# Kernel tuning notes

Measured on AMD Instinct MI355X. Metric: run time of the kernel, lower is better.

## Reference

```python
import jax, jax.numpy as jnp
import numpy as np

DIM = 256
NUM_HEADS = 8


def setup_inputs() -> dict:
    key = jax.random.key(0)
    ks = jax.random.split(key, 8)
    B, H, W = 2, 64, 64
    s = 0.02
    return {
        "query": jax.random.normal(ks[0], (B, H, W, DIM), jnp.float32),
        "sim": jax.random.normal(ks[1], (B, H, W, DIM), jnp.float32),
        "Wq": jax.random.normal(ks[2], (DIM, DIM), jnp.float32) * s,
        "bq": jnp.zeros((DIM,), jnp.float32),
        "Wkv": jax.random.normal(ks[3], (DIM, 2 * DIM), jnp.float32) * s,
        "bkv": jnp.zeros((2 * DIM,), jnp.float32),
        "Wp": jax.random.normal(ks[4], (DIM, DIM), jnp.float32) * s,
        "bp": jnp.zeros((DIM,), jnp.float32),
    }


def reference(query, sim, Wq, bq, Wkv, bkv, Wp, bp):
    B, H, W, dim = query.shape
    nh = NUM_HEADS
    dh = dim // nh
    scale = dh ** (-0.5)
    S = H * W

    # projections
    q = (query.reshape(B, S, dim) @ Wq + bq).reshape(B, S, nh, dh)
    kv = (sim.reshape(B, S, dim) @ Wkv + bkv).reshape(B, S, 2, nh, dh)
    k = kv[:, :, 0]  # [B,S,nh,dh]
    v = kv[:, :, 1]

    # attention: scores [B,nh,S,S]
    attn = jnp.einsum('bqhd,bkhd->bhqk', q * scale, k)
    attn = jax.nn.softmax(attn, axis=-1)
    x = jnp.einsum('bhqk,bkhd->bqhd', attn, v)  # [B,S,nh,dh]
    x = x.reshape(B, H, W, dim)
    return x @ Wp + bp
```

## Files before the change

kernel.cpp:

```cpp
#include <hip/hip_runtime.h>
#include <hip/hip_bf16.h>
#include <math.h>


#define SCALE 0.17677669529663687f
#define LOG2E 1.4426950408889634f

typedef __attribute__((ext_vector_type(8))) short short8;
typedef __attribute__((ext_vector_type(8))) _Float16 half8;
typedef __attribute__((ext_vector_type(4))) float f32x4;

static __device__ __forceinline__ unsigned short f2bf(float x) {
    union { float f; unsigned int u; } v; v.f = x;
    unsigned int r = v.u + 0x7fff + ((v.u >> 16) & 1);
    return (unsigned short)(r >> 16);
}
static __device__ __forceinline__ float bf2f(unsigned short h) {
    union { unsigned int u; float f; } v; v.u = ((unsigned int)h) << 16;
    return v.f;
}
static __device__ __forceinline__ float fexp2(float x) {
#if __has_builtin(__builtin_amdgcn_exp2f)
    return __builtin_amdgcn_exp2f(x);
#else
    float r; asm("v_exp_f32 %0, %1" : "=v"(r) : "v"(x)); return r;
#endif
}
static __device__ __forceinline__ unsigned int pk_bf16(float a, float b) {
    unsigned int r;
    asm("v_cvt_pk_bf16_f32 %0, %1, %2" : "=v"(r) : "v"(a), "v"(b));
    return r;
}
static __device__ __forceinline__ unsigned short f2h(float x) {
    _Float16 h = (_Float16)x;
    union { _Float16 h; unsigned short s; } u; u.h = h;
    return u.s;
}
static __device__ __forceinline__ float h2f(unsigned short s) {
    union { _Float16 h; unsigned short s; } u; u.s = s;
    return (float)u.h;
}

__global__ __launch_bounds__(256) void prep(
    const float* __restrict__ query, const float* __restrict__ sim,
    const float* __restrict__ Wq, const float* __restrict__ Wkv,
    const float* __restrict__ Wp,
    unsigned short* __restrict__ xhi, unsigned short* __restrict__ xlo,
    unsigned short* __restrict__ wfp)
{
    __shared__ float T[64][68];
    const int blk = blockIdx.x, t = threadIdx.x;
    if (blk < 4096) {
        const int e = blk * 1024 + t * 4;
        const float* src = (e < 2097152) ? (query + e) : (sim + (e - 2097152));
        float4 v = *(const float4*)src;
        float xv[4] = {v.x, v.y, v.z, v.w};
        union { unsigned short s[4]; uint2 u; } ph, pl;
#pragma unroll
        for (int j = 0; j < 4; ++j) {
            unsigned short h = f2h(xv[j]);
            ph.s[j] = h;
            pl.s[j] = f2h(xv[j] - h2f(h));
        }
        *(uint2*)&xhi[e] = ph.u;
        *(uint2*)&xlo[e] = pl.u;
        return;
    }
    const int bb = blk - 4096;
    const int mat = bb >> 4, tile = bb & 15;
    const int kr0 = (tile >> 2) * 64;
    const int nc0 = (tile & 3) * 64;
    const float* src; int ldw, cb; float sc = 1.f;
    if (mat == 0)      { src = Wq;  ldw = 256; cb = 0;   sc = SCALE * LOG2E; }
    else if (mat == 1) { src = Wkv; ldw = 512; cb = 0;   }
    else if (mat == 2) { src = Wkv; ldw = 512; cb = 256; }
    else               { src = Wp;  ldw = 256; cb = 0;   }
    {
        const int rl = t >> 4, c4 = (t & 15) * 4;
#pragma unroll
        for (int rr = 0; rr < 4; ++rr) {
            float4 v = *(const float4*)&src[(long long)(kr0 + rr * 16 + rl) * ldw + cb + nc0 + c4];
            T[rr * 16 + rl][c4 + 0] = v.x; T[rr * 16 + rl][c4 + 1] = v.y;
            T[rr * 16 + rl][c4 + 2] = v.z; T[rr * 16 + rl][c4 + 3] = v.w;
        }
    }
    __syncthreads();
    {
        const int nl = t >> 2, kl0 = (t & 3) * 16;
        const long long orow = (long long)(mat * 256 + nc0 + nl) * 256 + kr0 + kl0;
        union { unsigned short s[16]; uint4 u[2]; } ph;
#pragma unroll
        for (int j = 0; j < 16; ++j)
            ph.s[j] = f2h(T[kl0 + j][nl] * sc);
        *(uint4*)&wfp[orow] = ph.u[0];
        *(uint4*)&wfp[orow + 8] = ph.u[1];
    }
}

__global__ __launch_bounds__(256) void gemm_qkv(
    const unsigned short* __restrict__ xhi, const unsigned short* __restrict__ xlo,
    const unsigned short* __restrict__ wfp,
    const float* __restrict__ bq, const float* __restrict__ bkv,
    unsigned short* __restrict__ qbuf, unsigned short* __restrict__ kbuf,
    unsigned short* __restrict__ vTb)
{
    __shared__ unsigned short XsH[64 * 40], XsL[64 * 40], Ws[64 * 40];

    const int t = threadIdx.x, wave = t >> 6, lane = t & 63;
    const int col = lane & 15, quad = lane >> 4;
    const int by = blockIdx.y;
    const int kind = by >> 2;
    const int n0 = (by & 3) * 64;
    const int m0 = blockIdx.x * 64;
    const int xrow0 = ((kind == 0) ? 0 : 8192) + m0;
    const int wrow0 = kind * 256 + n0;
    const int srow = t >> 2, spart = (t & 3) * 8;

    const f32x4 zero = {0.f, 0.f, 0.f, 0.f};
    f32x4 acc[4] = {zero, zero, zero, zero};

    for (int kt = 0; kt < 8; ++kt) {
        const int k0 = kt * 32;
        uint4 xh = *(const uint4*)&xhi[(long long)(xrow0 + srow) * 256 + k0 + spart];
        uint4 xl = *(const uint4*)&xlo[(long long)(xrow0 + srow) * 256 + k0 + spart];
        uint4 wh = *(const uint4*)&wfp[(long long)(wrow0 + srow) * 256 + k0 + spart];
        __syncthreads();
        *(uint4*)&XsH[srow * 40 + spart] = xh;
        *(uint4*)&XsL[srow * 40 + spart] = xl;
        *(uint4*)&Ws[srow * 40 + spart] = wh;
        __syncthreads();

        if (kind < 2) {
            half8 a_h = *(const half8*)(XsH + (wave * 16 + col) * 40 + quad * 8);
            half8 a_l = *(const half8*)(XsL + (wave * 16 + col) * 40 + quad * 8);
#pragma unroll
            for (int nt = 0; nt < 4; ++nt) {
                half8 b = *(const half8*)(Ws + (nt * 16 + col) * 40 + quad * 8);
                acc[nt] = __builtin_amdgcn_mfma_f32_16x16x32_f16(a_h, b, acc[nt], 0, 0, 0);
                acc[nt] = __builtin_amdgcn_mfma_f32_16x16x32_f16(a_l, b, acc[nt], 0, 0, 0);
            }
        } else {
            half8 a = *(const half8*)(Ws + (wave * 16 + col) * 40 + quad * 8);
#pragma unroll
            for (int nt = 0; nt < 4; ++nt) {
                half8 b_h = *(const half8*)(XsH + (nt * 16 + col) * 40 + quad * 8);
                half8 b_l = *(const half8*)(XsL + (nt * 16 + col) * 40 + quad * 8);
                acc[nt] = __builtin_amdgcn_mfma_f32_16x16x32_f16(a, b_h, acc[nt], 0, 0, 0);
                acc[nt] = __builtin_amdgcn_mfma_f32_16x16x32_f16(a, b_l, acc[nt], 0, 0, 0);
            }
        }
    }

    if (kind == 0) {
#pragma unroll
        for (int nt = 0; nt < 4; ++nt) {
            int n = n0 + nt * 16 + col;
            int h = n >> 5, d = n & 31;
            float bias = bq[n] * (SCALE * LOG2E);
#pragma unroll
            for (int r = 0; r < 4; ++r) {
                int mg = m0 + wave * 16 + quad * 4 + r;
                int b = mg >> 12, sidx = mg & 4095;
                qbuf[((long long)(b * 8 + h) * 4096 + sidx) * 32 + d] = f2bf(acc[nt][r] + bias);
            }
        }
    } else if (kind == 1) {
#pragma unroll
        for (int nt = 0; nt < 4; ++nt) {
            int n = n0 + nt * 16 + col;
            int h = n >> 5, d = n & 31;
            float bias = bkv[n];
#pragma unroll
            for (int r = 0; r < 4; ++r) {
                int mg = m0 + wave * 16 + quad * 4 + r;
                int b = mg >> 12, sidx = mg & 4095;
                kbuf[((long long)(b * 8 + h) * 4096 + sidx) * 32 + d] = f2bf(acc[nt][r] + bias);
            }
        }
    } else {
#pragma unroll
        for (int nt = 0; nt < 4; ++nt) {
            int s = m0 + nt * 16 + col;
            int b = s >> 12, sidx = s & 4095;
#pragma unroll
            for (int r = 0; r < 4; ++r) {
                int dcol = n0 + wave * 16 + quad * 4 + r;
                int h = dcol >> 5, dd = dcol & 31;
                float bias = bkv[256 + dcol];
                vTb[((long long)((b * 8 + h) * 32 + dd)) * 4096 + sidx] = f2bf(acc[nt][r] + bias);
            }
        }
    }
}

__global__ __launch_bounds__(256) void flash_mfma(
    const unsigned short* __restrict__ qbuf,
    const unsigned short* __restrict__ kbuf,
    const unsigned short* __restrict__ vT,
    float* __restrict__ xpart, float* __restrict__ lpart)
{
    __shared__ unsigned short Ks[128 * 40];
    __shared__ unsigned short Vt[32 * 136];
    __shared__ unsigned short Pb[8][640];

    const int t = threadIdx.x;
    const int wave = t >> 6, lane = t & 63;
    const int col = lane & 15, quad = lane >> 4;
    const int qb = blockIdx.x & 31;
    const int bh = (blockIdx.x >> 5) & 15;
    const int ks = blockIdx.x >> 9;
    const int q0 = qb * 128 + wave * 32;
    const long long kvbase = (long long)bh * 4096 * 32;
    unsigned short* pb0 = Pb[wave * 2];
    unsigned short* pb1 = Pb[wave * 2 + 1];

    const short8 qf0 = *(const short8*)(qbuf + kvbase + (long long)(q0 + col) * 32 + quad * 8);
    const short8 qf1 = *(const short8*)(qbuf + kvbase + (long long)(q0 + 16 + col) * 32 + quad * 8);

    const f32x4 zero = {0.f, 0.f, 0.f, 0.f};
    f32x4 o00 = zero, o01 = zero, o10 = zero, o11 = zero;
    float l0 = 0.f, l1 = 0.f;

    const int krow = t >> 2, kpart = (t & 3) * 8;
    const int vrow = t >> 4, vpart = (t & 15) * 8;

    for (int kt0 = 0; kt0 < 16; ++kt0) {
        const int kt = ks * 16 + kt0;
        uint4 kg0 = *(const uint4*)(kbuf + kvbase + (long long)(kt * 128 + krow) * 32 + kpart);
        uint4 kg1 = *(const uint4*)(kbuf + kvbase + (long long)(kt * 128 + krow + 64) * 32 + kpart);
        uint4 vg0 = *(const uint4*)(vT + ((long long)(bh * 32 + vrow)) * 4096 + kt * 128 + vpart);
        uint4 vg1 = *(const uint4*)(vT + ((long long)(bh * 32 + vrow + 16)) * 4096 + kt * 128 + vpart);
        __syncthreads();
        *(uint4*)(Ks + krow * 40 + kpart) = kg0;
        *(uint4*)(Ks + (krow + 64) * 40 + kpart) = kg1;
        *(uint4*)(Vt + vrow * 136 + vpart) = vg0;
        *(uint4*)(Vt + (vrow + 16) * 136 + vpart) = vg1;
        __syncthreads();

#pragma unroll
        for (int sb = 0; sb < 4; ++sb) {
            const int kb = sb * 32;
            short8 a0 = *(const short8*)(Ks + (kb + col) * 40 + quad * 8);
            short8 a1 = *(const short8*)(Ks + (kb + 16 + col) * 40 + quad * 8);
            short8 v0 = *(const short8*)(Vt + col * 136 + kb + quad * 8);
            short8 v1 = *(const short8*)(Vt + (16 + col) * 136 + kb + quad * 8);
            {
                f32x4 c0 = __builtin_amdgcn_mfma_f32_16x16x32_bf16(a0, qf0, zero, 0, 0, 0);
                f32x4 c1 = __builtin_amdgcn_mfma_f32_16x16x32_bf16(a1, qf0, zero, 0, 0, 0);
                float p0 = fexp2(c0[0]), p1 = fexp2(c0[1]), p2 = fexp2(c0[2]), p3 = fexp2(c0[3]);
                float p4 = fexp2(c1[0]), p5 = fexp2(c1[1]), p6 = fexp2(c1[2]), p7 = fexp2(c1[3]);
                l0 += ((p0 + p1) + (p2 + p3)) + ((p4 + p5) + (p6 + p7));
                uint2 w0 = make_uint2(pk_bf16(p0, p1), pk_bf16(p2, p3));
                uint2 w1 = make_uint2(pk_bf16(p4, p5), pk_bf16(p6, p7));
                *(uint2*)(pb0 + col * 40 + quad * 4) = w0;
                *(uint2*)(pb0 + col * 40 + 16 + quad * 4) = w1;
                short8 pf = *(const short8*)(pb0 + col * 40 + quad * 8);
                o00 = __builtin_amdgcn_mfma_f32_16x16x32_bf16(v0, pf, o00, 0, 0, 0);
                o01 = __builtin_amdgcn_mfma_f32_16x16x32_bf16(v1, pf, o01, 0, 0, 0);
            }
            {
                f32x4 c0 = __builtin_amdgcn_mfma_f32_16x16x32_bf16(a0, qf1, zero, 0, 0, 0);
                f32x4 c1 = __builtin_amdgcn_mfma_f32_16x16x32_bf16(a1, qf1, zero, 0, 0, 0);
                float p0 = fexp2(c0[0]), p1 = fexp2(c0[1]), p2 = fexp2(c0[2]), p3 = fexp2(c0[3]);
                float p4 = fexp2(c1[0]), p5 = fexp2(c1[1]), p6 = fexp2(c1[2]), p7 = fexp2(c1[3]);
                l1 += ((p0 + p1) + (p2 + p3)) + ((p4 + p5) + (p6 + p7));
                uint2 w0 = make_uint2(pk_bf16(p0, p1), pk_bf16(p2, p3));
                uint2 w1 = make_uint2(pk_bf16(p4, p5), pk_bf16(p6, p7));
                *(uint2*)(pb1 + col * 40 + quad * 4) = w0;
                *(uint2*)(pb1 + col * 40 + 16 + quad * 4) = w1;
                short8 pf = *(const short8*)(pb1 + col * 40 + quad * 8);
                o10 = __builtin_amdgcn_mfma_f32_16x16x32_bf16(v0, pf, o10, 0, 0, 0);
                o11 = __builtin_amdgcn_mfma_f32_16x16x32_bf16(v1, pf, o11, 0, 0, 0);
            }
        }
    }

    l0 += __shfl_xor(l0, 16, 64); l0 += __shfl_xor(l0, 32, 64);
    l1 += __shfl_xor(l1, 16, 64); l1 += __shfl_xor(l1, 32, 64);

    const int b = bh >> 3, hh = bh & 7;
    float* xp = xpart + (long long)ks * 2097152;
    float* r0p = xp + ((long long)(b * 4096 + q0 + col)) * 256 + hh * 32;
    *(float4*)(r0p + quad * 4)      = make_float4(o00[0], o00[1], o00[2], o00[3]);
    *(float4*)(r0p + 16 + quad * 4) = make_float4(o01[0], o01[1], o01[2], o01[3]);
    float* r1p = xp + ((long long)(b * 4096 + q0 + 16 + col)) * 256 + hh * 32;
    *(float4*)(r1p + quad * 4)      = make_float4(o10[0], o10[1], o10[2], o10[3]);
    *(float4*)(r1p + 16 + quad * 4) = make_float4(o11[0], o11[1], o11[2], o11[3]);

    if (quad == 0)      lpart[ks * 65536 + bh * 4096 + q0 + col] = l0;
    else if (quad == 1) lpart[ks * 65536 + bh * 4096 + q0 + 16 + col] = l1;
}

__global__ __launch_bounds__(256) void gemm_outp(
    const float* __restrict__ xpart, const float* __restrict__ lpart,
    const unsigned short* __restrict__ wfp,
    const float* __restrict__ bp, float* __restrict__ out)
{
    __shared__ unsigned short XsH[64 * 40], XsL[64 * 40], Ws[64 * 40];

    const int t = threadIdx.x, wave = t >> 6, lane = t & 63;
    const int col = lane & 15, quad = lane >> 4;
    const int n0 = blockIdx.y * 64;
    const int m0 = blockIdx.x * 64;
    const int wrow0 = 768 + n0;
    const int srow = t >> 2, spart = (t & 3) * 8;
    const int r = m0 + srow;
    const int bidx = r >> 12, s = r & 4095;
    const float* __restrict__ xa = xpart;
    const float* __restrict__ xb = xpart + 2097152;

    const f32x4 zero = {0.f, 0.f, 0.f, 0.f};
    f32x4 acc[4] = {zero, zero, zero, zero};

    for (int kt = 0; kt < 8; ++kt) {
        const int k0 = kt * 32;
        const int head = k0 >> 5;
        float la = lpart[(bidx * 8 + head) * 4096 + s];
        float lb = lpart[65536 + (bidx * 8 + head) * 4096 + s];
        float linv = 1.f / (la + lb);
        const float* pa = &xa[(long long)r * 256 + k0 + spart];
        const float* pb = &xb[(long long)r * 256 + k0 + spart];
        float4 a0 = *(const float4*)pa, a1 = *(const float4*)(pa + 4);
        float4 b0 = *(const float4*)pb, b1 = *(const float4*)(pb + 4);
        float xv[8] = {(a0.x + b0.x) * linv, (a0.y + b0.y) * linv,
                       (a0.z + b0.z) * linv, (a0.w + b0.w) * linv,
                       (a1.x + b1.x) * linv, (a1.y + b1.y) * linv,
                       (a1.z + b1.z) * linv, (a1.w + b1.w) * linv};
        union { unsigned short s4[8]; uint4 u; } ph, pl;
#pragma unroll
        for (int j = 0; j < 8; ++j) {
            unsigned short h = f2h(xv[j]);
            ph.s4[j] = h;
            pl.s4[j] = f2h(xv[j] - h2f(h));
        }
        uint4 wh = *(const uint4*)&wfp[(long long)(wrow0 + srow) * 256 + k0 + spart];
        __syncthreads();
        *(uint4*)&XsH[srow * 40 + spart] = ph.u;
        *(uint4*)&XsL[srow * 40 + spart] = pl.u;
        *(uint4*)&Ws[srow * 40 + spart] = wh;
        __syncthreads();

        half8 a_h = *(const half8*)(XsH + (wave * 16 + col) * 40 + quad * 8);
        half8 a_l = *(const half8*)(XsL + (wave * 16 + col) * 40 + quad * 8);
#pragma unroll
        for (int nt = 0; nt < 4; ++nt) {
            half8 b = *(const half8*)(Ws + (nt * 16 + col) * 40 + quad * 8);
            acc[nt] = __builtin_amdgcn_mfma_f32_16x16x32_f16(a_h, b, acc[nt], 0, 0, 0);
            acc[nt] = __builtin_amdgcn_mfma_f32_16x16x32_f16(a_l, b, acc[nt], 0, 0, 0);
        }
    }

#pragma unroll
    for (int nt = 0; nt < 4; ++nt) {
        int n = n0 + nt * 16 + col;
        float bias = bp[n];
#pragma unroll
        for (int rr = 0; rr < 4; ++rr) {
            int mg = m0 + wave * 16 + quad * 4 + rr;
            out[(long long)mg * 256 + n] = acc[nt][rr] + bias;
        }
    }
}

extern "C" void kernel_launch(void* const* d_in, const int* in_sizes, int n_in,
                              void* d_out, int out_size, void* d_ws, size_t ws_size,
                              hipStream_t stream) {
    const float* query = (const float*)d_in[0];
    const float* sim   = (const float*)d_in[1];
    const float* Wq    = (const float*)d_in[2];
    const float* bq    = (const float*)d_in[3];
    const float* Wkv   = (const float*)d_in[4];
    const float* bkv   = (const float*)d_in[5];
    const float* Wp    = (const float*)d_in[6];
    const float* bp    = (const float*)d_in[7];
    float* out = (float*)d_out;

    unsigned short* wsb = (unsigned short*)d_ws;
    unsigned short* qbuf = wsb;
    unsigned short* kbuf = wsb + 2097152;
    unsigned short* vT   = wsb + 4194304;
    unsigned short* wfp  = wsb + 6291456;
    unsigned short* xhi  = wsb + 6553600;
    unsigned short* xlo  = wsb + 10747904;
    float* xpart = (float*)(wsb + 6553600);
    float* lpart = (float*)(wsb + 14942208);

    prep      <<<dim3(4160),    256, 0, stream>>>(query, sim, Wq, Wkv, Wp,
                                                  xhi, xlo, wfp);
    gemm_qkv  <<<dim3(128, 12), 256, 0, stream>>>(xhi, xlo, wfp, bq, bkv,
                                                  qbuf, kbuf, vT);
    flash_mfma<<<dim3(1024),    256, 0, stream>>>(qbuf, kbuf, vT, xpart, lpart);
    gemm_outp <<<dim3(128, 4),  256, 0, stream>>>(xpart, lpart, wfp, bp, out);
}
```

Baseline: 166.7 us.

## Fuse fp16 activation conversion into QKV GEMM and drop split-precision low part

The prep kernel no longer converts query/sim into hi/lo fp16 pairs. The QKV GEMM now loads fp32 activations directly and converts them to fp16 on the fly, and it issues one MFMA per tile instead of two because the lo-part correction is gone. This removes a full pass over the inputs, one intermediate buffer's traffic and half the projection MFMAs, at the cost of fp16 rounding error on the activations. Separately, the V-transpose LDS row stride in the flash kernel changes from 136 to 152, apparently to reduce bank conflicts.

```diff
diff --git a/kernel.cpp b/kernel.cpp
--- a/kernel.cpp
+++ b/kernel.cpp
@@ -42,31 +42,11 @@
 }
 
 __global__ __launch_bounds__(256) void prep(
-    const float* __restrict__ query, const float* __restrict__ sim,
     const float* __restrict__ Wq, const float* __restrict__ Wkv,
-    const float* __restrict__ Wp,
-    unsigned short* __restrict__ xhi, unsigned short* __restrict__ xlo,
-    unsigned short* __restrict__ wfp)
+    const float* __restrict__ Wp, unsigned short* __restrict__ wfp)
 {
     __shared__ float T[64][68];
-    const int blk = blockIdx.x, t = threadIdx.x;
-    if (blk < 4096) {
-        const int e = blk * 1024 + t * 4;
-        const float* src = (e < 2097152) ? (query + e) : (sim + (e - 2097152));
-        float4 v = *(const float4*)src;
-        float xv[4] = {v.x, v.y, v.z, v.w};
-        union { unsigned short s[4]; uint2 u; } ph, pl;
-#pragma unroll
-        for (int j = 0; j < 4; ++j) {
-            unsigned short h = f2h(xv[j]);
-            ph.s[j] = h;
-            pl.s[j] = f2h(xv[j] - h2f(h));
-        }
-        *(uint2*)&xhi[e] = ph.u;
-        *(uint2*)&xlo[e] = pl.u;
-        return;
-    }
-    const int bb = blk - 4096;
+    const int bb = blockIdx.x, t = threadIdx.x;
     const int mat = bb >> 4, tile = bb & 15;
     const int kr0 = (tile >> 2) * 64;
     const int nc0 = (tile & 3) * 64;
@@ -98,13 +78,13 @@
 }
 
 __global__ __launch_bounds__(256) void gemm_qkv(
-    const unsigned short* __restrict__ xhi, const unsigned short* __restrict__ xlo,
+    const float* __restrict__ query, const float* __restrict__ sim,
     const unsigned short* __restrict__ wfp,
     const float* __restrict__ bq, const float* __restrict__ bkv,
     unsigned short* __restrict__ qbuf, unsigned short* __restrict__ kbuf,
     unsigned short* __restrict__ vTb)
 {
-    __shared__ unsigned short XsH[64 * 40], XsL[64 * 40], Ws[64 * 40];
+    __shared__ unsigned short Xs[64 * 40], Ws[64 * 40];
 
     const int t = threadIdx.x, wave = t >> 6, lane = t & 63;
     const int col = lane & 15, quad = lane >> 4;
@@ -112,7 +92,7 @@
     const int kind = by >> 2;
     const int n0 = (by & 3) * 64;
     const int m0 = blockIdx.x * 64;
-    const int xrow0 = ((kind == 0) ? 0 : 8192) + m0;
+    const float* __restrict__ X = (kind == 0) ? query : sim;
     const int wrow0 = kind * 256 + n0;
     const int srow = t >> 2, spart = (t & 3) * 8;
 
@@ -121,32 +101,32 @@
 
     for (int kt = 0; kt < 8; ++kt) {
         const int k0 = kt * 32;
-        uint4 xh = *(const uint4*)&xhi[(long long)(xrow0 + srow) * 256 + k0 + spart];
-        uint4 xl = *(const uint4*)&xlo[(long long)(xrow0 + srow) * 256 + k0 + spart];
+        const float* xp = &X[(long long)(m0 + srow) * 256 + k0 + spart];
+        float4 xa = *(const float4*)xp;
+        float4 xb = *(const float4*)(xp + 4);
+        float xv[8] = {xa.x, xa.y, xa.z, xa.w, xb.x, xb.y, xb.z, xb.w};
+        union { unsigned short s[8]; uint4 u; } ph;
+#pragma unroll
+        for (int j = 0; j < 8; ++j) ph.s[j] = f2h(xv[j]);
         uint4 wh = *(const uint4*)&wfp[(long long)(wrow0 + srow) * 256 + k0 + spart];
         __syncthreads();
-        *(uint4*)&XsH[srow * 40 + spart] = xh;
-        *(uint4*)&XsL[srow * 40 + spart] = xl;
+        *(uint4*)&Xs[srow * 40 + spart] = ph.u;
         *(uint4*)&Ws[srow * 40 + spart] = wh;
         __syncthreads();
 
         if (kind < 2) {
-            half8 a_h = *(const half8*)(XsH + (wave * 16 + col) * 40 + quad * 8);
-            half8 a_l = *(const half8*)(XsL + (wave * 16 + col) * 40 + quad * 8);
+            half8 a = *(const half8*)(Xs + (wave * 16 + col) * 40 + quad * 8);
 #pragma unroll
             for (int nt = 0; nt < 4; ++nt) {
                 half8 b = *(const half8*)(Ws + (nt * 16 + col) * 40 + quad * 8);
-                acc[nt] = __builtin_amdgcn_mfma_f32_16x16x32_f16(a_h, b, acc[nt], 0, 0, 0);
-                acc[nt] = __builtin_amdgcn_mfma_f32_16x16x32_f16(a_l, b, acc[nt], 0, 0, 0);
+                acc[nt] = __builtin_amdgcn_mfma_f32_16x16x32_f16(a, b, acc[nt], 0, 0, 0);
             }
         } else {
             half8 a = *(const half8*)(Ws + (wave * 16 + col) * 40 + quad * 8);
 #pragma unroll
             for (int nt = 0; nt < 4; ++nt) {
-                half8 b_h = *(const half8*)(XsH + (nt * 16 + col) * 40 + quad * 8);
-                half8 b_l = *(const half8*)(XsL + (nt * 16 + col) * 40 + quad * 8);
-                acc[nt] = __builtin_amdgcn_mfma_f32_16x16x32_f16(a, b_h, acc[nt], 0, 0, 0);
-                acc[nt] = __builtin_amdgcn_mfma_f32_16x16x32_f16(a, b_l, acc[nt], 0, 0, 0);
+                half8 b = *(const half8*)(Xs + (nt * 16 + col) * 40 + quad * 8);
+                acc[nt] = __builtin_amdgcn_mfma_f32_16x16x32_f16(a, b, acc[nt], 0, 0, 0);
             }
         }
     }
@@ -200,7 +180,7 @@
     float* __restrict__ xpart, float* __restrict__ lpart)
 {
     __shared__ unsigned short Ks[128 * 40];
-    __shared__ unsigned short Vt[32 * 136];
+    __shared__ unsigned short Vt[32 * 152];
     __shared__ unsigned short Pb[8][640];
 
     const int t = threadIdx.x;
@@ -233,8 +213,8 @@
         __syncthreads();
         *(uint4*)(Ks + krow * 40 + kpart) = kg0;
         *(uint4*)(Ks + (krow + 64) * 40 + kpart) = kg1;
-        *(uint4*)(Vt + vrow * 136 + vpart) = vg0;
-        *(uint4*)(Vt + (vrow + 16) * 136 + vpart) = vg1;
+        *(uint4*)(Vt + vrow * 152 + vpart) = vg0;
+        *(uint4*)(Vt + (vrow + 16) * 152 + vpart) = vg1;
         __syncthreads();
 
 #pragma unroll
@@ -242,8 +222,8 @@
             const int kb = sb * 32;
             short8 a0 = *(const short8*)(Ks + (kb + col) * 40 + quad * 8);
             short8 a1 = *(const short8*)(Ks + (kb + 16 + col) * 40 + quad * 8);
-            short8 v0 = *(const short8*)(Vt + col * 136 + kb + quad * 8);
-            short8 v1 = *(const short8*)(Vt + (16 + col) * 136 + kb + quad * 8);
+            short8 v0 = *(const short8*)(Vt + col * 152 + kb + quad * 8);
+            short8 v1 = *(const short8*)(Vt + (16 + col) * 152 + kb + quad * 8);
             {
                 f32x4 c0 = __builtin_amdgcn_mfma_f32_16x16x32_bf16(a0, qf0, zero, 0, 0, 0);
                 f32x4 c1 = __builtin_amdgcn_mfma_f32_16x16x32_bf16(a1, qf0, zero, 0, 0, 0);
@@ -380,14 +360,11 @@
     unsigned short* kbuf = wsb + 2097152;
     unsigned short* vT   = wsb + 4194304;
     unsigned short* wfp  = wsb + 6291456;
-    unsigned short* xhi  = wsb + 6553600;
-    unsigned short* xlo  = wsb + 10747904;
     float* xpart = (float*)(wsb + 6553600);
     float* lpart = (float*)(wsb + 14942208);
 
-    prep      <<<dim3(4160),    256, 0, stream>>>(query, sim, Wq, Wkv, Wp,
-                                                  xhi, xlo, wfp);
-    gemm_qkv  <<<dim3(128, 12), 256, 0, stream>>>(xhi, xlo, wfp, bq, bkv,
+    prep      <<<dim3(64),      256, 0, stream>>>(Wq, Wkv, Wp, wfp);
+    gemm_qkv  <<<dim3(128, 12), 256, 0, stream>>>(query, sim, wfp, bq, bkv,
                                                   qbuf, kbuf, vT);
     flash_mfma<<<dim3(1024),    256, 0, stream>>>(qbuf, kbuf, vT, xpart, lpart);
     gemm_outp <<<dim3(128, 4),  256, 0, stream>>>(xpart, lpart, wfp, bp, out);
```

Measured after the change: 158.9 us. 1.05x faster.
